# Performance work log

Measured on AMD Instinct MI355X. Metric: run time of the kernel, lower is better.

The kernel has to match this reference:

```python
import jax, jax.numpy as jnp
import numpy as np

B, T, F, U, M = 4096, 16, 256, 512, 8
DELTA_T = 0.04

# ln_tau_table: tau = 1, 10^0.5, 10^1.0, ... -> ln(tau) = i * 0.5*ln(10)
LN_TAU = (jnp.arange(M, dtype=jnp.float32) * (0.5 * np.log(10.0))).astype(jnp.float32)
DECAY = jnp.exp(-DELTA_T / (LN_TAU + 1e-7))  # [M]


def setup_inputs() -> dict:
    key = jax.random.key(0)
    ks = jax.random.split(key, 9)
    s = lambda fan_in: 1.0 / np.sqrt(fan_in)
    return {
        "x": jax.random.normal(ks[0], (B, T, F), dtype=jnp.float32),
        "W_r": jax.random.normal(ks[1], (F + U, U * M), dtype=jnp.float32) * s(F + U),
        "b_r": jax.random.normal(ks[2], (U * M,), dtype=jnp.float32) * 0.01,
        "W_q": jax.random.normal(ks[3], (F + U, U), dtype=jnp.float32) * s(F + U),
        "b_q": jax.random.normal(ks[4], (U,), dtype=jnp.float32) * 0.01,
        "W_s": jax.random.normal(ks[5], (F + U, U * M), dtype=jnp.float32) * s(F + U),
        "b_s": jax.random.normal(ks[6], (U * M,), dtype=jnp.float32) * 0.01,
        "W_out": jax.random.normal(ks[7], (U, 3), dtype=jnp.float32) * s(U),
        "b_out": jax.random.normal(ks[8], (3,), dtype=jnp.float32) * 0.01,
    }


def _ctgru_forward(x, W_r, b_r, W_q, b_q, W_s, b_s, W_out, b_out):
    def step(h_hat, x_t):  # h_hat: [B,U,M], x_t: [B,F]
        h = h_hat.sum(axis=2)                              # [B,U]
        fused = jnp.concatenate([x_t, h], axis=1)          # [B,F+U]
        ln_tau_r = (fused @ W_r + b_r).reshape(-1, U, M)   # [B,U,M]
        r_ki = jax.nn.softmax(-jnp.square(ln_tau_r - LN_TAU), axis=2)
        q_in = jnp.concatenate([x_t, jnp.sum(r_ki * h_hat, axis=2)], axis=1)
        q_k = jnp.tanh(q_in @ W_q + b_q)[:, :, None]       # [B,U,1]
        ln_tau_s = (fused @ W_s + b_s).reshape(-1, U, M)
        s_ki = jax.nn.softmax(-jnp.square(ln_tau_s - LN_TAU), axis=2)
        h_next = ((1.0 - s_ki) * h_hat + s_ki * q_k) * DECAY
        return h_next, h_next.sum(axis=2)                  # carry, hidden [B,U]

    h0 = jnp.zeros((x.shape[0], U, M), dtype=x.dtype)
    _, hiddens = jax.lax.scan(step, h0, jnp.swapaxes(x, 0, 1))  # hiddens: [T,B,U]
    outputs = jnp.swapaxes(hiddens, 0, 1)                  # [B,T,U]
    return outputs @ W_out + b_out                         # [B,T,3]


def reference(x, W_r, b_r, W_q, b_q, W_s, b_s, W_out, b_out):
    return _ctgru_forward(x, W_r, b_r, W_q, b_q, W_s, b_s, W_out, b_out)
```

## Files before the change

### kernel.cpp

```cpp
#include <hip/hip_runtime.h>
#include <hip/hip_bf16.h>
#include <math.h>

#define B_   4096
#define T_   16
#define F_   256
#define U_   512
#define M_   8
#define K_   768
#define NRS  4096
#define NC   8192
#define LNT  1.1512925f

#define XPH  32768
#define XPT  1048576
#define HPH  65536
#define BPH  98304
#define QPP  12288

typedef __bf16 bf16_t;
typedef bf16_t bf16x8 __attribute__((ext_vector_type(8)));
typedef bf16_t bf16x4 __attribute__((ext_vector_type(4)));
typedef float  f32x4  __attribute__((ext_vector_type(4)));

__device__ inline void gl_lds16(const void* g, void* lds) {
    __builtin_amdgcn_global_load_lds(
        (const __attribute__((address_space(1))) unsigned int*)g,
        (__attribute__((address_space(3))) unsigned int*)lds, 16, 0, 0);
}

#define VMCNT(n) asm volatile("s_waitcnt vmcnt(" #n ")" ::: "memory")
#define LGKM0()  asm volatile("s_waitcnt lgkmcnt(0)" ::: "memory")
#define BAR()    __builtin_amdgcn_s_barrier()

__device__ inline void stage8(const bf16_t* src, bf16_t* dst, int tid) {
    gl_lds16(src + tid * 8,        (char*)dst + tid * 16);
    gl_lds16(src + tid * 8 + 2048, (char*)dst + tid * 16 + 4096);
}

__global__ __launch_bounds__(256, 4) void gemm_r(
    const bf16_t* __restrict__ xt_t,
    const bf16_t* __restrict__ ht,
    const bf16_t* __restrict__ Bt,
    const float*  __restrict__ biasP,
    const bf16_t* __restrict__ hhat,
    bf16_t* __restrict__ rh)
{
    __shared__ __attribute__((aligned(16))) bf16_t Ahl[2][4096];
    __shared__ __attribute__((aligned(16))) bf16_t Bhl[2][4096];

    const int tid  = threadIdx.x;
    const int lane = tid & 63;
    const int wave = tid >> 6;

    const int lin = blockIdx.y * 32 + blockIdx.x;
    const int c = lin & 7, q = lin >> 3;
    const int mh = (c >> 1) * 8 + (q & 7);
    const int nh = (c & 1) * 16 + (q >> 3);
    const int m0 = mh * 128;
    const int NH = nh;

    const int wm = wave >> 1;
    const int wn = wave & 1;
    const int lr = lane & 15;
    const int kq = lane >> 4;

    const bf16_t* xp = xt_t + (size_t)mh * XPH;
    const bf16_t* hp = ht   + (size_t)mh * HPH;
    const bf16_t* bp = Bt   + (size_t)NH * BPH;

    const int aoff = kq * 1024 + (wm * 64 + lr) * 8;
    const int boff = kq * 1024 + (wn * 64 + lr) * 8;

    f32x4 acc[4][4] = {};

    stage8(xp, &Ahl[0][0], tid);
    stage8(bp, &Bhl[0][0], tid);
    VMCNT(0);
    BAR();

#pragma unroll
    for (int tt = 0; tt < 24; ++tt) {
        const int p = tt & 1, pn = p ^ 1;
        if (tt < 23) {
            const bf16_t* as = (tt + 1 < 8) ? xp + (tt + 1) * 4096
                                            : hp + (tt + 1 - 8) * 4096;
            stage8(as, &Ahl[pn][0], tid);
            stage8(bp + (tt + 1) * 4096, &Bhl[pn][0], tid);
        }
        bf16x8 a[4], b[4];
#pragma unroll
        for (int i = 0; i < 4; ++i)
            a[i] = *(const bf16x8*)(&Ahl[p][0] + aoff + i * 128);
#pragma unroll
        for (int j = 0; j < 4; ++j)
            b[j] = *(const bf16x8*)(&Bhl[p][0] + boff + j * 128);
        LGKM0();
        __builtin_amdgcn_s_setprio(1);
#pragma unroll
        for (int i = 0; i < 4; ++i)
#pragma unroll
            for (int j = 0; j < 4; ++j)
                acc[i][j] = __builtin_amdgcn_mfma_f32_16x16x32_bf16(
                    a[i], b[j], acc[i][j], 0, 0, 0);
        __builtin_amdgcn_s_setprio(0);
        VMCNT(0);
        BAR();
    }

    const int nb  = NH * 128 + wn * 64;
    const int u3  = lane & 7;
    const int m0v = ((lane >> 3) & 1) * 4;

    float bj4[4];
#pragma unroll
    for (int j = 0; j < 4; ++j) bj4[j] = biasP[nb + j * 16 + lr];

#pragma unroll
    for (int mi = 0; mi < 4; ++mi) {
        const int rowb = m0 + wm * 64 + mi * 16 + kq * 4;
#pragma unroll
        for (int r = 0; r < 4; ++r) {
            const int row = rowb + r;
            float e[4], sum = 0.f;
#pragma unroll
            for (int j = 0; j < 4; ++j) {
                float v = acc[mi][j][r] + bj4[j];
                float d = v - (float)(m0v + j) * LNT;
                e[j] = __expf(-d * d);
                sum += e[j];
            }
            sum += __shfl_xor(sum, 8, 64);
            const float inv = 1.0f / sum;
            bf16x4 h4 = *(const bf16x4*)(hhat + (size_t)row * NRS + nb + u3 * 8 + m0v);
            float rhv = 0.f;
#pragma unroll
            for (int j = 0; j < 4; ++j) rhv += e[j] * inv * (float)h4[j];
            rhv += __shfl_xor(rhv, 8, 64);
            if ((lane & 8) == 0)
                rh[(size_t)row * U_ + (nb >> 3) + u3] = (bf16_t)rhv;
        }
    }
}

template <int FIRST>
__global__ __launch_bounds__(256, 4) void gemm_sq(
    const bf16_t* __restrict__ xt_t,
    const bf16_t* __restrict__ htr,
    const bf16_t* __restrict__ Bt,
    const float*  __restrict__ biasP,
    const bf16_t* __restrict__ rh,
    const bf16_t* __restrict__ Bq16,
    const float*  __restrict__ bq,
    bf16_t* __restrict__ hhat,
    bf16_t* __restrict__ hnext,
    bf16_t* __restrict__ htw)
{
    __shared__ __attribute__((aligned(16))) bf16_t Ahl[2][4096];
    __shared__ __attribute__((aligned(16))) bf16_t Bhl[2][4096];
    __shared__ __attribute__((aligned(16))) float  qls[2048];

    const int tid  = threadIdx.x;
    const int lane = tid & 63;
    const int wave = tid >> 6;

    const int lin = blockIdx.y * 32 + blockIdx.x;
    const int c = lin & 7, qq = lin >> 3;
    const int mh = (c >> 1) * 8 + (qq & 7);
    const int nh = (c & 1) * 16 + (qq >> 3);
    const int m0 = mh * 128;
    const int NH = 32 + nh;

    const int wm = wave >> 1;
    const int wn = wave & 1;
    const int lr = lane & 15;
    const int kq = lane >> 4;

    const bf16_t* xp = xt_t + (size_t)mh * XPH;
    const bf16_t* hp = htr  + (size_t)mh * HPH;
    const bf16_t* bp = Bt   + (size_t)NH * BPH;
    const bf16_t* bqp = Bq16 + (size_t)nh * QPP;

    const int NT = FIRST ? 8 : 24;

    {
        f32x4 accq[2] = {};
        const bf16_t* bqk = bqp + kq * 128 + lr * 8;
        const bf16_t* xf  = xp + kq * 1024 + (wave * 32 + lr) * 8;
#pragma unroll
        for (int kt = 0; kt < 8; ++kt) {
            bf16x8 bqf = *(const bf16x8*)(bqk + kt * 512);
            bf16x8 a0  = *(const bf16x8*)(xf + kt * 4096);
            bf16x8 a1  = *(const bf16x8*)(xf + kt * 4096 + 128);
            accq[0] = __builtin_amdgcn_mfma_f32_16x16x32_bf16(a0, bqf, accq[0], 0, 0, 0);
            accq[1] = __builtin_amdgcn_mfma_f32_16x16x32_bf16(a1, bqf, accq[1], 0, 0, 0);
        }
        if (!FIRST) {
            const bf16_t* rf0 = rh + (size_t)(m0 + wave * 32 + lr) * U_ + kq * 8;
            const bf16_t* rf1 = rf0 + (size_t)16 * U_;
#pragma unroll
            for (int kt = 0; kt < 16; ++kt) {
                bf16x8 bqf = *(const bf16x8*)(bqk + (8 + kt) * 512);
                bf16x8 a0  = *(const bf16x8*)(rf0 + kt * 32);
                bf16x8 a1  = *(const bf16x8*)(rf1 + kt * 32);
                accq[0] = __builtin_amdgcn_mfma_f32_16x16x32_bf16(a0, bqf, accq[0], 0, 0, 0);
                accq[1] = __builtin_amdgcn_mfma_f32_16x16x32_bf16(a1, bqf, accq[1], 0, 0, 0);
            }
        }
        const float bqv = bq[nh * 16 + lr];
#pragma unroll
        for (int i = 0; i < 2; ++i)
#pragma unroll
            for (int r = 0; r < 4; ++r)
                qls[(wave * 32 + i * 16 + kq * 4 + r) * 16 + lr] =
                    tanhf(accq[i][r] + bqv);
    }
    BAR();

    const int aoff = kq * 1024 + (wm * 64 + lr) * 8;
    const int boff = kq * 1024 + (wn * 64 + lr) * 8;

    f32x4 acc[4][4] = {};

    stage8(xp, &Ahl[0][0], tid);
    stage8(bp, &Bhl[0][0], tid);
    VMCNT(0);
    BAR();

#pragma unroll
    for (int tt = 0; tt < NT; ++tt) {
        const int p = tt & 1, pn = p ^ 1;
        if (tt < NT - 1) {
            const bf16_t* as = (tt + 1 < 8) ? xp + (tt + 1) * 4096
                                            : hp + (tt + 1 - 8) * 4096;
            stage8(as, &Ahl[pn][0], tid);
            stage8(bp + (tt + 1) * 4096, &Bhl[pn][0], tid);
        }
        bf16x8 a[4], b[4];
#pragma unroll
        for (int i = 0; i < 4; ++i)
            a[i] = *(const bf16x8*)(&Ahl[p][0] + aoff + i * 128);
#pragma unroll
        for (int j = 0; j < 4; ++j)
            b[j] = *(const bf16x8*)(&Bhl[p][0] + boff + j * 128);
        LGKM0();
        __builtin_amdgcn_s_setprio(1);
#pragma unroll
        for (int i = 0; i < 4; ++i)
#pragma unroll
            for (int j = 0; j < 4; ++j)
                acc[i][j] = __builtin_amdgcn_mfma_f32_16x16x32_bf16(
                    a[i], b[j], acc[i][j], 0, 0, 0);
        __builtin_amdgcn_s_setprio(0);
        VMCNT(0);
        BAR();
    }

    const int nb  = NH * 128 + wn * 64;
    const int u3  = lane & 7;
    const int m0v = ((lane >> 3) & 1) * 4;
    const int hcol = nh * 128 + wn * 64;

    const float DECL[4] = {0.0f, 0.9658531f, 0.9827783f, 0.9884856f};
    const float DECH[4] = {0.9913518f, 0.9930754f, 0.9942261f, 0.9950489f};

    float bj4[4];
#pragma unroll
    for (int j = 0; j < 4; ++j) bj4[j] = biasP[nb + j * 16 + lr];

#pragma unroll
    for (int mi = 0; mi < 4; ++mi) {
        const int rowb = m0 + wm * 64 + mi * 16 + kq * 4;
        const int rlb  = wm * 64 + mi * 16 + kq * 4;
#pragma unroll
        for (int r = 0; r < 4; ++r) {
            const int row = rowb + r;
            float e[4], sum = 0.f;
#pragma unroll
            for (int j = 0; j < 4; ++j) {
                float v = acc[mi][j][r] + bj4[j];
                float d = v - (float)(m0v + j) * LNT;
                e[j] = __expf(-d * d);
                sum += e[j];
            }
            sum += __shfl_xor(sum, 8, 64);
            const float inv = 1.0f / sum;
            const float qv = qls[(rlb + r) * 16 + wn * 8 + u3];

            const size_t ha = (size_t)row * NRS + hcol + u3 * 8 + m0v;
            bf16x4 h4;
            if (!FIRST) h4 = *(const bf16x4*)(hhat + ha);
            bf16x4 ho;
            float hs = 0.f;
#pragma unroll
            for (int j = 0; j < 4; ++j) {
                float s = e[j] * inv;
                float h = FIRST ? 0.f : (float)h4[j];
                float dec = m0v ? DECH[j] : DECL[j];
                float hn = ((1.f - s) * h + s * qv) * dec;
                ho[j] = (bf16_t)hn;
                hs += hn;
            }
            *(bf16x4*)(hhat + ha) = ho;
            hs += __shfl_xor(hs, 8, 64);
            if ((lane & 8) == 0) {
                const int u = nh * 16 + wn * 8 + u3;
                hnext[(size_t)row * U_ + u] = (bf16_t)hs;
                htw[((size_t)(row >> 7) * 16 + (u >> 5)) * 4096
                    + ((((u >> 3) & 3) * 128) + (row & 127)) * 8 + (u & 7)] = (bf16_t)hs;
            }
        }
    }
}

__global__ void transpose_perm(const float* __restrict__ src, bf16_t* __restrict__ dst) {
    __shared__ float tl[32][33];
    int k0 = blockIdx.x * 32, n0 = blockIdx.y * 32;
    int tx = threadIdx.x & 31, ty = threadIdx.x >> 5;
#pragma unroll
    for (int i = 0; i < 32; i += 8)
        tl[ty + i][tx] = src[(size_t)(k0 + ty + i) * NRS + n0 + tx];
    __syncthreads();
#pragma unroll
    for (int i = 0; i < 32; i += 8) {
        int n = n0 + ty + i;
        int m = n & 7, u3v = (n >> 3) & 7;
        int p = (n & ~63) + (m & 3) * 16 + (m >> 2) * 8 + u3v;
        dst[(size_t)p * K_ + k0 + tx] = (bf16_t)tl[tx][ty + i];
    }
}

__global__ void btile_build(const bf16_t* __restrict__ WrsT, bf16_t* __restrict__ Bt) {
    int n = blockIdx.x / 3;
    int k = (blockIdx.x % 3) * 256 + threadIdx.x;
    int NH = n >> 7, prow = n & 127;
    int kt = k >> 5, ch = (k >> 3) & 3, e = k & 7;
    Bt[(size_t)NH * BPH + (((size_t)kt * 4 + ch) * 128 + prow) * 8 + e]
        = WrsT[(size_t)n * K_ + k];
}

__global__ void bq16_build(const float* __restrict__ Wq, bf16_t* __restrict__ Bq16) {
    int i = blockIdx.x * 256 + threadIdx.x;
    int k = i >> 9, u = i & 511;
    int nh = u >> 4, ul = u & 15;
    int kt = k >> 5, ch = (k >> 3) & 3, e = k & 7;
    Bq16[(size_t)nh * QPP + ((size_t)kt * 4 + ch) * 128 + ul * 8 + e] = (bf16_t)Wq[i];
}

__global__ void bias_perm(const float* __restrict__ b_r, const float* __restrict__ b_s,
                          float* __restrict__ biasP) {
    int p = blockIdx.x * 256 + threadIdx.x;
    int pr = p & 63, j = pr >> 4, lr = pr & 15;
    int L = (p & ~63) + (lr & 7) * 8 + ((lr >> 3) & 1) * 4 + j;
    biasP[p] = (L < NRS) ? b_r[L] : b_s[L - NRS];
}

__global__ void xtile_build(const float* __restrict__ x, bf16_t* __restrict__ xt) {
    int idx = blockIdx.x * 256 + threadIdx.x;
    int b = idx >> 9;
    int rem = idx & 511;
    int t = rem >> 5, c8 = rem & 31;
    int f0 = c8 * 8;
    const float* src = x + ((size_t)b * T_ + t) * F_ + f0;
    float4 v0 = *(const float4*)(src);
    float4 v1 = *(const float4*)(src + 4);
    bf16x8 o;
    o[0] = (bf16_t)v0.x; o[1] = (bf16_t)v0.y; o[2] = (bf16_t)v0.z; o[3] = (bf16_t)v0.w;
    o[4] = (bf16_t)v1.x; o[5] = (bf16_t)v1.y; o[6] = (bf16_t)v1.z; o[7] = (bf16_t)v1.w;
    int mh = b >> 7, prow = b & 127;
    int kt = f0 >> 5, ch = (f0 >> 3) & 3;
    *(bf16x8*)(xt + (size_t)t * XPT + (size_t)mh * XPH
               + (((size_t)kt * 4 + ch) * 128 + prow) * 8) = o;
}

__global__ __launch_bounds__(256) void out_all(
    const bf16_t* __restrict__ hall,
    const float* __restrict__ Wout,
    const float* __restrict__ bout,
    float* __restrict__ out)
{
    int row = blockIdx.x * 4 + (threadIdx.x >> 6);
    int lane = threadIdx.x & 63;
    bf16x8 h8 = *(const bf16x8*)(hall + (size_t)row * U_ + lane * 8);
    float p0 = 0, p1 = 0, p2 = 0;
#pragma unroll
    for (int k = 0; k < 8; k++) {
        float h = (float)h8[k];
        int u = lane * 8 + k;
        p0 += h * Wout[u * 3 + 0];
        p1 += h * Wout[u * 3 + 1];
        p2 += h * Wout[u * 3 + 2];
    }
    for (int off = 32; off; off >>= 1) {
        p0 += __shfl_down(p0, off, 64);
        p1 += __shfl_down(p1, off, 64);
        p2 += __shfl_down(p2, off, 64);
    }
    if (lane == 0) {
        int t = row >> 12, b = row & (B_ - 1);
        size_t o = ((size_t)b * T_ + t) * 3;
        out[o + 0] = p0 + bout[0];
        out[o + 1] = p1 + bout[1];
        out[o + 2] = p2 + bout[2];
    }
}

extern "C" void kernel_launch(void* const* d_in, const int* in_sizes, int n_in,
                              void* d_out, int out_size, void* d_ws, size_t ws_size,
                              hipStream_t stream) {
    const float* x   = (const float*)d_in[0];
    const float* W_r = (const float*)d_in[1];
    const float* b_r = (const float*)d_in[2];
    const float* W_q = (const float*)d_in[3];
    const float* b_q = (const float*)d_in[4];
    const float* W_s = (const float*)d_in[5];
    const float* b_s = (const float*)d_in[6];
    const float* W_o = (const float*)d_in[7];
    const float* b_o = (const float*)d_in[8];
    float* out = (float*)d_out;

    char* ws = (char*)d_ws;
    bf16_t* hhat  = (bf16_t*)ws; ws += (size_t)B_ * NRS * 2;
    bf16_t* xtile = (bf16_t*)ws; ws += (size_t)T_ * XPT * 2;
    bf16_t* hall  = (bf16_t*)ws; ws += (size_t)(T_ + 1) * B_ * U_ * 2;
    bf16_t* rh    = (bf16_t*)ws; ws += (size_t)B_ * U_ * 2;
    bf16_t* WrsT  = (bf16_t*)ws; ws += (size_t)NC * K_ * 2;
    bf16_t* Btile = (bf16_t*)ws; ws += (size_t)NC * K_ * 2;
    bf16_t* htA   = (bf16_t*)ws; ws += (size_t)32 * HPH * 2;
    bf16_t* htB   = (bf16_t*)ws; ws += (size_t)32 * HPH * 2;
    bf16_t* Bq16  = (bf16_t*)ws; ws += (size_t)32 * QPP * 2;
    float*  biasP = (float*)ws;  ws += (size_t)NC * 4;

    xtile_build<<<B_ * T_ * F_ / 8 / 256, 256, 0, stream>>>(x, xtile);
    transpose_perm<<<dim3(K_ / 32, NRS / 32), 256, 0, stream>>>(W_r, WrsT);
    transpose_perm<<<dim3(K_ / 32, NRS / 32), 256, 0, stream>>>(W_s, WrsT + (size_t)NRS * K_);
    btile_build<<<NC * 3, 256, 0, stream>>>(WrsT, Btile);
    bq16_build<<<K_ * U_ / 256, 256, 0, stream>>>(W_q, Bq16);
    bias_perm<<<NC / 256, 256, 0, stream>>>(b_r, b_s, biasP);

    bf16_t* htbuf[2] = {htA, htB};
    for (int t = 0; t < T_; t++) {
        const bf16_t* xt_t = xtile + (size_t)t * XPT;
        const bf16_t* htr  = htbuf[t & 1];
        bf16_t*       htw  = htbuf[(t + 1) & 1];
        bf16_t*       hn   = hall + (size_t)(t + 1) * B_ * U_;
        if (t == 0) {
            gemm_sq<1><<<dim3(32, 32), 256, 0, stream>>>(
                xt_t, htr, Btile, biasP, rh, Bq16, b_q, hhat, hn, htw);
        } else {
            gemm_r<<<dim3(32, 32), 256, 0, stream>>>(
                xt_t, htr, Btile, biasP, hhat, rh);
            gemm_sq<0><<<dim3(32, 32), 256, 0, stream>>>(
                xt_t, htr, Btile, biasP, rh, Bq16, b_q, hhat, hn, htw);
        }
    }
    out_all<<<B_ * T_ / 4, 256, 0, stream>>>(hall + (size_t)B_ * U_, W_o, b_o, out);
}
```

Before: 1.523 ms.

## Load B operand directly from global into registers, double-buffered, skipping LDS

The B (weight) tiles in both GEMM kernels are now read straight from global memory into registers with a two-set ping-pong (b0/b1). They are no longer staged through LDS. The wait before each barrier changes from vmcnt(0) to vmcnt(4), so next-tile B loads can stay in flight across the barrier while only A goes through LDS. This removes half the LDS traffic and LDS footprint, possibly raising occupancy. In exchange it adds VGPR pressure and depends on the vmcnt ordering being right for the LDS-bound A loads.

```diff
diff --git a/kernel.cpp b/kernel.cpp
--- a/kernel.cpp
+++ b/kernel.cpp
@@ -38,6 +38,35 @@
     gl_lds16(src + tid * 8 + 2048, (char*)dst + tid * 16 + 4096);
 }
 
+#define KLOOP_DEFS                                                             \
+  f32x4 acc[4][4] = {};                                                        \
+  bf16x8 b0[4], b1[4];
+
+#define LDBG(D, T) do{ const bf16_t* _p = bp + (size_t)(T) * 4096 + bgo;       \
+    D[0] = *(const bf16x8*)(_p);       D[1] = *(const bf16x8*)(_p + 128);      \
+    D[2] = *(const bf16x8*)(_p + 256); D[3] = *(const bf16x8*)(_p + 384); }while(0)
+
+#define KTILE(T, NT, BC, BN)                                                   \
+  {                                                                            \
+    const int p_ = (T) & 1, pn_ = p_ ^ 1;                                      \
+    if ((T) < (NT) - 1) {                                                      \
+      stage8(ASRC((T) + 1), &Ahl[pn_][0], tid);                                \
+      LDBG(BN, (T) + 1);                                                       \
+    }                                                                          \
+    bf16x8 a_[4];                                                              \
+    _Pragma("unroll") for (int i_ = 0; i_ < 4; ++i_)                           \
+        a_[i_] = *(const bf16x8*)(&Ahl[p_][0] + aoff + i_ * 128);              \
+    LGKM0();                                                                   \
+    __builtin_amdgcn_s_setprio(1);                                             \
+    _Pragma("unroll") for (int i_ = 0; i_ < 4; ++i_)                           \
+      _Pragma("unroll") for (int j_ = 0; j_ < 4; ++j_)                         \
+        acc[i_][j_] = __builtin_amdgcn_mfma_f32_16x16x32_bf16(                 \
+            a_[i_], BC[j_], acc[i_][j_], 0, 0, 0);                             \
+    __builtin_amdgcn_s_setprio(0);                                             \
+    if ((T) < (NT) - 1) VMCNT(4);                                              \
+    BAR();                                                                     \
+  }
+
 __global__ __launch_bounds__(256, 4) void gemm_r(
     const bf16_t* __restrict__ xt_t,
     const bf16_t* __restrict__ ht,
@@ -47,7 +76,6 @@
     bf16_t* __restrict__ rh)
 {
     __shared__ __attribute__((aligned(16))) bf16_t Ahl[2][4096];
-    __shared__ __attribute__((aligned(16))) bf16_t Bhl[2][4096];
 
     const int tid  = threadIdx.x;
     const int lane = tid & 63;
@@ -70,43 +98,21 @@
     const bf16_t* bp = Bt   + (size_t)NH * BPH;
 
     const int aoff = kq * 1024 + (wm * 64 + lr) * 8;
-    const int boff = kq * 1024 + (wn * 64 + lr) * 8;
-
-    f32x4 acc[4][4] = {};
-
-    stage8(xp, &Ahl[0][0], tid);
-    stage8(bp, &Bhl[0][0], tid);
-    VMCNT(0);
+    const int bgo  = kq * 1024 + (wn * 64 + lr) * 8;
+
+    KLOOP_DEFS
+
+#define ASRC(T) (((T) < 8) ? xp + (T) * 4096 : hp + ((T) - 8) * 4096)
+    stage8(ASRC(0), &Ahl[0][0], tid);
+    LDBG(b0, 0);
+    VMCNT(4);
     BAR();
-
-#pragma unroll
-    for (int tt = 0; tt < 24; ++tt) {
-        const int p = tt & 1, pn = p ^ 1;
-        if (tt < 23) {
-            const bf16_t* as = (tt + 1 < 8) ? xp + (tt + 1) * 4096
-                                            : hp + (tt + 1 - 8) * 4096;
-            stage8(as, &Ahl[pn][0], tid);
-            stage8(bp + (tt + 1) * 4096, &Bhl[pn][0], tid);
-        }
-        bf16x8 a[4], b[4];
-#pragma unroll
-        for (int i = 0; i < 4; ++i)
-            a[i] = *(const bf16x8*)(&Ahl[p][0] + aoff + i * 128);
-#pragma unroll
-        for (int j = 0; j < 4; ++j)
-            b[j] = *(const bf16x8*)(&Bhl[p][0] + boff + j * 128);
-        LGKM0();
-        __builtin_amdgcn_s_setprio(1);
-#pragma unroll
-        for (int i = 0; i < 4; ++i)
-#pragma unroll
-            for (int j = 0; j < 4; ++j)
-                acc[i][j] = __builtin_amdgcn_mfma_f32_16x16x32_bf16(
-                    a[i], b[j], acc[i][j], 0, 0, 0);
-        __builtin_amdgcn_s_setprio(0);
-        VMCNT(0);
-        BAR();
-    }
+#pragma unroll
+    for (int tt = 0; tt < 24; tt += 2) {
+        KTILE(tt, 24, b0, b1);
+        KTILE(tt + 1, 24, b1, b0);
+    }
+#undef ASRC
 
     const int nb  = NH * 128 + wn * 64;
     const int u3  = lane & 7;
@@ -157,7 +163,6 @@
     bf16_t* __restrict__ htw)
 {
     __shared__ __attribute__((aligned(16))) bf16_t Ahl[2][4096];
-    __shared__ __attribute__((aligned(16))) bf16_t Bhl[2][4096];
     __shared__ __attribute__((aligned(16))) float  qls[2048];
 
     const int tid  = threadIdx.x;
@@ -180,8 +185,6 @@
     const bf16_t* hp = htr  + (size_t)mh * HPH;
     const bf16_t* bp = Bt   + (size_t)NH * BPH;
     const bf16_t* bqp = Bq16 + (size_t)nh * QPP;
-
-    const int NT = FIRST ? 8 : 24;
 
     {
         f32x4 accq[2] = {};
@@ -218,43 +221,30 @@
     BAR();
 
     const int aoff = kq * 1024 + (wm * 64 + lr) * 8;
-    const int boff = kq * 1024 + (wn * 64 + lr) * 8;
-
-    f32x4 acc[4][4] = {};
-
-    stage8(xp, &Ahl[0][0], tid);
-    stage8(bp, &Bhl[0][0], tid);
+    const int bgo  = kq * 1024 + (wn * 64 + lr) * 8;
+
+    KLOOP_DEFS
+
+#define ASRC(T) (((T) < 8) ? xp + (T) * 4096 : hp + ((T) - 8) * 4096)
     VMCNT(0);
+    stage8(ASRC(0), &Ahl[0][0], tid);
+    LDBG(b0, 0);
+    VMCNT(4);
     BAR();
-
-#pragma unroll
-    for (int tt = 0; tt < NT; ++tt) {
-        const int p = tt & 1, pn = p ^ 1;
-        if (tt < NT - 1) {
-            const bf16_t* as = (tt + 1 < 8) ? xp + (tt + 1) * 4096
-                                            : hp + (tt + 1 - 8) * 4096;
-            stage8(as, &Ahl[pn][0], tid);
-            stage8(bp + (tt + 1) * 4096, &Bhl[pn][0], tid);
-        }
-        bf16x8 a[4], b[4];
-#pragma unroll
-        for (int i = 0; i < 4; ++i)
-            a[i] = *(const bf16x8*)(&Ahl[p][0] + aoff + i * 128);
-#pragma unroll
-        for (int j = 0; j < 4; ++j)
-            b[j] = *(const bf16x8*)(&Bhl[p][0] + boff + j * 128);
-        LGKM0();
-        __builtin_amdgcn_s_setprio(1);
-#pragma unroll
-        for (int i = 0; i < 4; ++i)
-#pragma unroll
-            for (int j = 0; j < 4; ++j)
-                acc[i][j] = __builtin_amdgcn_mfma_f32_16x16x32_bf16(
-                    a[i], b[j], acc[i][j], 0, 0, 0);
-        __builtin_amdgcn_s_setprio(0);
-        VMCNT(0);
-        BAR();
-    }
+    if (FIRST) {
+#pragma unroll
+        for (int tt = 0; tt < 8; tt += 2) {
+            KTILE(tt, 8, b0, b1);
+            KTILE(tt + 1, 8, b1, b0);
+        }
+    } else {
+#pragma unroll
+        for (int tt = 0; tt < 24; tt += 2) {
+            KTILE(tt, 24, b0, b1);
+            KTILE(tt + 1, 24, b1, b0);
+        }
+    }
+#undef ASRC
 
     const int nb  = NH * 128 + wn * 64;
     const int u3  = lane & 7;
```

After: 1.520 ms. About the same (-0.2%).
